# Kernel optimization log

Measured on AMD Instinct MI355X. Metric: run time of the kernel, lower is better.

## Reference

```python
import jax, jax.numpy as jnp
import numpy as np

B, N, M, D, NHEAD, FF, C, K = 2, 16384, 2048, 256, 8, 512, 50, 3
HID = 128          # embed/pos hidden
HEAD_HID = 256     # seg head hidden
L = 4              # depth
EPS = 1e-5


def setup_inputs() -> dict:
    key = jax.random.key(0)
    ks = jax.random.split(key, 32)
    g = lambda i, shape: jax.random.normal(ks[i], shape, dtype=jnp.float32) * 0.02
    z = lambda shape: jnp.zeros(shape, jnp.float32)
    o = lambda shape: jnp.ones(shape, jnp.float32)
    return {
        "xyz": jax.random.normal(ks[0], (B, N, 3), dtype=jnp.float32),
        "embed_w1": g(1, (3, HID)), "embed_b1": z((HID,)),
        "embed_w2": g(2, (HID, D)), "embed_b2": z((D,)),
        "pos_w1": g(3, (3, HID)), "pos_b1": z((HID,)),
        "pos_w2": g(4, (HID, D)), "pos_b2": z((D,)),
        "Wq": g(5, (L, D, D)), "bq": z((L, D)),
        "Wk": g(6, (L, D, D)), "bk": z((L, D)),
        "Wv": g(7, (L, D, D)), "bv": z((L, D)),
        "Wo": g(8, (L, D, D)), "bo": z((L, D)),
        "ln1_s": o((L, D)), "ln1_b": z((L, D)),
        "W1": g(9, (L, D, FF)), "b1": z((L, FF)),
        "W2": g(10, (L, FF, D)), "b2": z((L, D)),
        "ln2_s": o((L, D)), "ln2_b": z((L, D)),
        "head_w1": g(11, (D, HEAD_HID)), "head_b1": z((HEAD_HID,)),
        "head_w2": g(12, (HEAD_HID, C)), "head_b2": z((C,)),
    }


def _ln(x, s, b):
    m = x.mean(-1, keepdims=True)
    v = ((x - m) ** 2).mean(-1, keepdims=True)
    return (x - m) / jnp.sqrt(v + EPS) * s + b


def reference(xyz, embed_w1, embed_b1, embed_w2, embed_b2,
              pos_w1, pos_b1, pos_w2, pos_b2,
              Wq, bq, Wk, bk, Wv, bv, Wo, bo, ln1_s, ln1_b,
              W1, b1, W2, b2, ln2_s, ln2_b,
              head_w1, head_b1, head_w2, head_b2):
    # deterministic token subsample (replaces randperm stub): strided pick of M points
    stride = N // M
    tok = xyz[:, ::stride, :][:, :M]                                  # [B,M,3]
    # per-point embed + learned positional encoding
    x = jax.nn.relu(tok @ embed_w1 + embed_b1) @ embed_w2 + embed_b2  # [B,M,D]
    x = x + jax.nn.relu(tok @ pos_w1 + pos_b1) @ pos_w2 + pos_b2
    dh = D // NHEAD
    scale = 1.0 / jnp.sqrt(jnp.float32(dh))

    def layer(x, p):
        wq, bq_, wk, bk_, wv, bv_, wo, bo_, l1s, l1b, w1, b1_, w2, b2_, l2s, l2b = p
        # pre-norm MHSA
        y = _ln(x, l1s, l1b)
        q = (y @ wq + bq_).reshape(B, M, NHEAD, dh)
        k = (y @ wk + bk_).reshape(B, M, NHEAD, dh)
        v = (y @ wv + bv_).reshape(B, M, NHEAD, dh)
        att = jax.nn.softmax(jnp.einsum('bqhd,bkhd->bhqk', q, k) * scale, axis=-1)
        o = jnp.einsum('bhqk,bkhd->bqhd', att, v).reshape(B, M, D)
        x = x + o @ wo + bo_
        # pre-norm FFN (gelu, exact erf as in torch)
        y = _ln(x, l2s, l2b)
        x = x + jax.nn.gelu(y @ w1 + b1_, approximate=False) @ w2 + b2_
        return x, None

    x, _ = jax.lax.scan(layer, x, (Wq, bq, Wk, bk, Wv, bv, Wo, bo,
                                   ln1_s, ln1_b, W1, b1, W2, b2, ln2_s, ln2_b))
    logits_tok = jax.nn.relu(x @ head_w1 + head_b1) @ head_w2 + head_b2  # [B,M,C]

    # kNN propagation N->M: dist^2 = |q|^2 + |k|^2 - 2 q.k, topk smallest
    q2 = (xyz ** 2).sum(-1)[..., None]            # [B,N,1]
    k2 = (tok ** 2).sum(-1)[:, None, :]           # [B,1,M]
    dist = q2 + k2 - 2.0 * jnp.einsum('bnd,bmd->bnm', xyz, tok)
    dist = jax.lax.stop_gradient(jnp.maximum(dist, 0.0))
    idx = jax.lax.top_k(-dist, K)[1]              # [B,N,K]
    logits_nk = logits_tok[jnp.arange(B)[:, None, None], idx]  # [B,N,K,C]
    return logits_nk.mean(axis=2)                 # [B,N,C]
```

## Files before the change

kernel.cpp:

```cpp
#include <hip/hip_runtime.h>
#include <hip/hip_bf16.h>
#include <math.h>

#define B_ 2
#define N_ 16384
#define M_ 2048
#define D_ 256
#define NHEAD_ 8
#define DH_ 32
#define FF_ 512
#define C_ 50
#define HID_ 128
#define HHID_ 256
#define L_ 4
#define EPS_ 1e-5f
#define TOK_ (B_*M_)
#define QSCALE_ 0.25507604155757994f

typedef short short8 __attribute__((ext_vector_type(8)));
typedef short short4_t __attribute__((ext_vector_type(4)));
typedef float f32x4 __attribute__((ext_vector_type(4)));

__device__ __forceinline__ short f2bf(float f) {
  union { float f; unsigned u; } c; c.f = f;
  unsigned u = c.u;
  unsigned r = (u + 0x7FFFu + ((u >> 16) & 1u)) >> 16;
  return (short)r;
}
__device__ __forceinline__ float fast_exp2(float x) {
  float r;
  asm("v_exp_f32 %0, %1" : "=v"(r) : "v"(x));
  return r;
}
__device__ __forceinline__ unsigned cvt_pk_bf16(float lo, float hi) {
  unsigned r;
  asm("v_cvt_pk_bf16_f32 %0, %1, %2" : "=v"(r) : "v"(lo), "v"(hi));
  return r;
}
__device__ __forceinline__ float med3f(float a, float b, float c) {
  float r;
  asm("v_med3_f32 %0, %1, %2, %3" : "=v"(r) : "v"(a), "v"(b), "v"(c));
  return r;
}

__global__ __launch_bounds__(256) void wconv_all(
    const float* __restrict__ Wq, const float* __restrict__ Wk,
    const float* __restrict__ Wv, const float* __restrict__ Wo,
    const float* __restrict__ W1, const float* __restrict__ W2,
    const float* __restrict__ h1,
    short* __restrict__ WqT, short* __restrict__ WkT,
    short* __restrict__ WvT, short* __restrict__ WoT,
    short* __restrict__ W1T, short* __restrict__ W2T, short* __restrict__ h1T) {
  int bid = blockIdx.x;
  const float* W; short* WT; int Kd, Nd, tn, tk;
  if (bid < 256) {
    int mat = bid >> 6, rem = bid & 63, l = rem >> 4, t = rem & 15;
    W  = (mat == 0 ? Wq : mat == 1 ? Wk : mat == 2 ? Wv : Wo) + l * 65536;
    WT = (mat == 0 ? WqT : mat == 1 ? WkT : mat == 2 ? WvT : WoT) + l * 65536;
    Kd = 256; Nd = 256; tn = t & 3; tk = t >> 2;
  } else if (bid < 384) {
    int rem = bid - 256, l = rem >> 5, t = rem & 31;
    W = W1 + l * 131072; WT = W1T + l * 131072;
    Kd = 256; Nd = 512; tn = t & 7; tk = t >> 3;
  } else if (bid < 512) {
    int rem = bid - 384, l = rem >> 5, t = rem & 31;
    W = W2 + l * 131072; WT = W2T + l * 131072;
    Kd = 512; Nd = 256; tn = t & 3; tk = t >> 2;
  } else {
    int t = bid - 512;
    W = h1; WT = h1T; Kd = 256; Nd = 256; tn = t & 3; tk = t >> 2;
  }
  int n0 = tn * 64, k0 = tk * 64;
  __shared__ short ts[64][72];
  int tid = threadIdx.x;
  #pragma unroll
  for (int i = 0; i < 4; ++i) {
    int r = i * 16 + (tid >> 4);
    int c4 = (tid & 15) * 4;
    float4 v = *(const float4*)&W[(size_t)(k0 + r) * Nd + n0 + c4];
    ts[c4 + 0][r] = f2bf(v.x);
    ts[c4 + 1][r] = f2bf(v.y);
    ts[c4 + 2][r] = f2bf(v.z);
    ts[c4 + 3][r] = f2bf(v.w);
  }
  __syncthreads();
  #pragma unroll
  for (int i = 0; i < 2; ++i) {
    int n = i * 32 + (tid >> 3);
    int kc = (tid & 7) * 8;
    *(short8*)&WT[(size_t)(n0 + n) * Kd + k0 + kc] = *(short8*)&ts[n][kc];
  }
}

__global__ __launch_bounds__(128) void embed_kernel(
    const float* __restrict__ xyz,
    const float* __restrict__ ew1, const float* __restrict__ eb1,
    const float* __restrict__ ew2, const float* __restrict__ eb2,
    const float* __restrict__ pw1, const float* __restrict__ pb1,
    const float* __restrict__ pw2, const float* __restrict__ pb2,
    float* __restrict__ x) {
  int t = blockIdx.x;
  int b = t / M_, m = t % M_;
  const float* p = xyz + ((size_t)b * N_ + (size_t)m * 8) * 3;
  float t0 = p[0], t1 = p[1], t2 = p[2];
  __shared__ float he[HID_], hp[HID_];
  int j = threadIdx.x;
  {
    float a = fmaf(t0, ew1[j], fmaf(t1, ew1[HID_ + j], fmaf(t2, ew1[2 * HID_ + j], eb1[j])));
    he[j] = fmaxf(a, 0.f);
    float c = fmaf(t0, pw1[j], fmaf(t1, pw1[HID_ + j], fmaf(t2, pw1[2 * HID_ + j], pb1[j])));
    hp[j] = fmaxf(c, 0.f);
  }
  __syncthreads();
  for (int d = j; d < D_; d += HID_) {
    float acc = eb2[d] + pb2[d];
    for (int k = 0; k < HID_; ++k) {
      acc = fmaf(he[k], ew2[k * D_ + d], acc);
      acc = fmaf(hp[k], pw2[k * D_ + d], acc);
    }
    x[(size_t)t * D_ + d] = acc;
  }
}

__global__ __launch_bounds__(256) void ln_kernel(
    const float* __restrict__ x, const float* __restrict__ s,
    const float* __restrict__ bb, short* __restrict__ y16) {
  int r = blockIdx.x * 4 + (threadIdx.x >> 6);
  int t = threadIdx.x & 63;
  const float4* xr = (const float4*)(x + (size_t)r * D_);
  float4 v = xr[t];
  float sum = v.x + v.y + v.z + v.w;
  #pragma unroll
  for (int o = 1; o < 64; o <<= 1) sum += __shfl_xor(sum, o, 64);
  float mean = sum * (1.f / D_);
  float dx = v.x - mean, dy = v.y - mean, dz = v.z - mean, dw = v.w - mean;
  float vs = dx * dx + dy * dy + dz * dz + dw * dw;
  #pragma unroll
  for (int o = 1; o < 64; o <<= 1) vs += __shfl_xor(vs, o, 64);
  float inv = 1.0f / sqrtf(vs * (1.f / D_) + EPS_);
  float4 sv = ((const float4*)s)[t];
  float4 bv = ((const float4*)bb)[t];
  short4_t ov;
  ov[0] = f2bf(dx * inv * sv.x + bv.x);
  ov[1] = f2bf(dy * inv * sv.y + bv.y);
  ov[2] = f2bf(dz * inv * sv.z + bv.z);
  ov[3] = f2bf(dw * inv * sv.w + bv.w);
  *(short4_t*)(y16 + (size_t)r * D_ + t * 4) = ov;
}

__global__ __launch_bounds__(256) void head2_kernel(
    const float* __restrict__ y, const float* __restrict__ w2,
    const float* __restrict__ b2, float* __restrict__ lt) {
  __shared__ float ys[4][HHID_];
  int w = threadIdx.x >> 6, l = threadIdx.x & 63;
  int t = blockIdx.x * 4 + w;
  float4 v = ((const float4*)(y + (size_t)t * HHID_))[l];
  *(float4*)&ys[w][l * 4] = v;
  int c = l < C_ ? l : 0;
  float a0 = 0.f, a1 = 0.f, a2 = 0.f, a3 = 0.f;
  #pragma unroll 4
  for (int k = 0; k < HHID_; k += 4) {
    a0 = fmaf(ys[w][k + 0], w2[(k + 0) * C_ + c], a0);
    a1 = fmaf(ys[w][k + 1], w2[(k + 1) * C_ + c], a1);
    a2 = fmaf(ys[w][k + 2], w2[(k + 2) * C_ + c], a2);
    a3 = fmaf(ys[w][k + 3], w2[(k + 3) * C_ + c], a3);
  }
  if (l < C_) lt[(size_t)t * C_ + l] = (a0 + a1) + (a2 + a3) + b2[l];
}

template <int ACT, int RES>
__device__ __forceinline__ void gemm16_body(
    const short* __restrict__ A16, const short* __restrict__ WT,
    const float* __restrict__ bias, const float* __restrict__ R,
    float* __restrict__ C, short* __restrict__ C16, short* __restrict__ VT,
    float oscale, int K, int Ncols, int m0, int n0) {
  __shared__ short As[64][40];
  __shared__ short Bs[64][40];
  int tid = threadIdx.x;
  int w = tid >> 6, l = tid & 63;
  int lq = l & 15, lg = l >> 4;
  int wr = (w & 1) * 32, wc = (w >> 1) * 32;
  int sr = tid >> 2, sk = (tid & 3) * 8;
  f32x4 acc00 = {0.f, 0.f, 0.f, 0.f};
  f32x4 acc01 = {0.f, 0.f, 0.f, 0.f};
  f32x4 acc10 = {0.f, 0.f, 0.f, 0.f};
  f32x4 acc11 = {0.f, 0.f, 0.f, 0.f};
  for (int kk = 0; kk < K; kk += 32) {
    __syncthreads();
    *(short8*)&As[sr][sk] = *(const short8*)&A16[(size_t)(m0 + sr) * K + kk + sk];
    *(short8*)&Bs[sr][sk] = *(const short8*)&WT[(size_t)(n0 + sr) * K + kk + sk];
    __syncthreads();
    short8 a0 = *(short8*)&As[wr + lq][lg * 8];
    short8 a1 = *(short8*)&As[wr + 16 + lq][lg * 8];
    short8 b0 = *(short8*)&Bs[wc + lq][lg * 8];
    short8 b1 = *(short8*)&Bs[wc + 16 + lq][lg * 8];
    acc00 = __builtin_amdgcn_mfma_f32_16x16x32_bf16(a0, b0, acc00, 0, 0, 0);
    acc01 = __builtin_amdgcn_mfma_f32_16x16x32_bf16(a0, b1, acc01, 0, 0, 0);
    acc10 = __builtin_amdgcn_mfma_f32_16x16x32_bf16(a1, b0, acc10, 0, 0, 0);
    acc11 = __builtin_amdgcn_mfma_f32_16x16x32_bf16(a1, b1, acc11, 0, 0, 0);
  }
  #pragma unroll
  for (int fi = 0; fi < 2; ++fi) {
    int row = m0 + wr + fi * 16 + lg * 4;
    #pragma unroll
    for (int fj = 0; fj < 2; ++fj) {
      int col = n0 + wc + fj * 16 + lq;
      short4_t vt4;
      #pragma unroll
      for (int r = 0; r < 4; ++r) {
        float v = (fi == 0 ? (fj == 0 ? acc00[r] : acc01[r])
                           : (fj == 0 ? acc10[r] : acc11[r])) + bias[col];
        if (ACT == 1) v = fmaxf(v, 0.f);
        else if (ACT == 2) v = 0.5f * v * (1.f + erff(v * 0.70710678118654752f));
        if (RES) v += R[(size_t)(row + r) * Ncols + col];
        if (C)   C[(size_t)(row + r) * Ncols + col] = v;
        if (C16) C16[(size_t)(row + r) * Ncols + col] = f2bf(v * oscale);
        if (VT)  vt4[r] = f2bf(v);
      }
      if (VT) {
        int bb = row >> 11, mm = row & (M_ - 1);
        *(short4_t*)&VT[((size_t)(bb * 256 + col)) * M_ + mm] = vt4;
      }
    }
  }
}

template <int ACT, int RES>
__global__ __launch_bounds__(256) void gemm16(
    const short* __restrict__ A16, const short* __restrict__ WT,
    const float* __restrict__ bias, const float* __restrict__ R,
    float* __restrict__ C, short* __restrict__ C16,
    int K, int Ncols) {
  gemm16_body<ACT, RES>(A16, WT, bias, R, C, C16, nullptr, 1.f, K, Ncols,
                        blockIdx.y * 64, blockIdx.x * 64);
}

__global__ __launch_bounds__(256) void qkv16(
    const short* __restrict__ A16,
    const short* __restrict__ WqT, const short* __restrict__ WkT, const short* __restrict__ WvT,
    const float* __restrict__ bq, const float* __restrict__ bk, const float* __restrict__ bv,
    short* __restrict__ q16, short* __restrict__ k16, short* __restrict__ vt16) {
  int sel = blockIdx.x >> 2;
  int n0 = (blockIdx.x & 3) << 6;
  int m0 = blockIdx.y * 64;
  if (sel == 0) {
    gemm16_body<0, 0>(A16, WqT, bq, nullptr, nullptr, q16, nullptr, QSCALE_, D_, D_, m0, n0);
  } else if (sel == 1) {
    gemm16_body<0, 0>(A16, WkT, bk, nullptr, nullptr, k16, nullptr, 1.f, D_, D_, m0, n0);
  } else {
    gemm16_body<0, 0>(A16, WvT, bv, nullptr, nullptr, nullptr, vt16, 1.f, D_, D_, m0, n0);
  }
}

__global__ __launch_bounds__(256) void wo_gemm(
    const float* __restrict__ po0, const float* __restrict__ po1,
    const float* __restrict__ po2, const float* __restrict__ po3,
    const float* __restrict__ pl, const short* __restrict__ WT,
    const float* __restrict__ bias, float* __restrict__ X) {
  __shared__ short As[64][260];
  __shared__ short Bs[64][40];
  int tid = threadIdx.x;
  int w = tid >> 6, l = tid & 63;
  int m0 = blockIdx.y * 64, n0 = blockIdx.x * 64;
  #pragma unroll 4
  for (int c = 0; c < 16; ++c) {
    int t = w * 16 + c;
    int row = m0 + t;
    int bb = row >> 11, mm = row & (M_ - 1);
    int h = l >> 3, d0 = (l & 7) * 4;
    size_t f = (size_t)(bb * NHEAD_ + h) * M_ + mm;
    float inv = 1.f / (pl[f] + pl[16 * M_ + f] + pl[32 * M_ + f] + pl[48 * M_ + f]);
    float4 p0 = *(const float4*)&po0[f * 32 + d0];
    float4 p1 = *(const float4*)&po1[f * 32 + d0];
    float4 p2 = *(const float4*)&po2[f * 32 + d0];
    float4 p3 = *(const float4*)&po3[f * 32 + d0];
    short4_t s;
    s[0] = f2bf((p0.x + p1.x + p2.x + p3.x) * inv);
    s[1] = f2bf((p0.y + p1.y + p2.y + p3.y) * inv);
    s[2] = f2bf((p0.z + p1.z + p2.z + p3.z) * inv);
    s[3] = f2bf((p0.w + p1.w + p2.w + p3.w) * inv);
    *(short4_t*)&As[t][l * 4] = s;
  }
  int lq = l & 15, lg = l >> 4;
  int wr = (w & 1) * 32, wc = (w >> 1) * 32;
  int sr = tid >> 2, sk = (tid & 3) * 8;
  f32x4 acc00 = {0.f, 0.f, 0.f, 0.f};
  f32x4 acc01 = {0.f, 0.f, 0.f, 0.f};
  f32x4 acc10 = {0.f, 0.f, 0.f, 0.f};
  f32x4 acc11 = {0.f, 0.f, 0.f, 0.f};
  for (int kk = 0; kk < D_; kk += 32) {
    __syncthreads();
    *(short8*)&Bs[sr][sk] = *(const short8*)&WT[(size_t)(n0 + sr) * D_ + kk + sk];
    __syncthreads();
    short8 a0 = *(short8*)&As[wr + lq][kk + lg * 8];
    short8 a1 = *(short8*)&As[wr + 16 + lq][kk + lg * 8];
    short8 b0 = *(short8*)&Bs[wc + lq][lg * 8];
    short8 b1 = *(short8*)&Bs[wc + 16 + lq][lg * 8];
    acc00 = __builtin_amdgcn_mfma_f32_16x16x32_bf16(a0, b0, acc00, 0, 0, 0);
    acc01 = __builtin_amdgcn_mfma_f32_16x16x32_bf16(a0, b1, acc01, 0, 0, 0);
    acc10 = __builtin_amdgcn_mfma_f32_16x16x32_bf16(a1, b0, acc10, 0, 0, 0);
    acc11 = __builtin_amdgcn_mfma_f32_16x16x32_bf16(a1, b1, acc11, 0, 0, 0);
  }
  #pragma unroll
  for (int fi = 0; fi < 2; ++fi) {
    int row = m0 + wr + fi * 16 + lg * 4;
    #pragma unroll
    for (int fj = 0; fj < 2; ++fj) {
      int col = n0 + wc + fj * 16 + lq;
      #pragma unroll
      for (int r = 0; r < 4; ++r) {
        float v = (fi == 0 ? (fj == 0 ? acc00[r] : acc01[r])
                           : (fj == 0 ? acc10[r] : acc11[r])) + bias[col];
        v += X[(size_t)(row + r) * D_ + col];
        X[(size_t)(row + r) * D_ + col] = v;
      }
    }
  }
}

#define KSTR 40
#define VSTR 72
#define PSTR 72
__global__ __launch_bounds__(256) void attn_mfma_kernel(
    const short* __restrict__ q16, const short* __restrict__ k16,
    const short* __restrict__ vt16,
    float* __restrict__ po0, float* __restrict__ po1,
    float* __restrict__ po2, float* __restrict__ po3,
    float* __restrict__ pl) {
  __shared__ short Ks[64][KSTR];
  __shared__ short Vt[32][VSTR];
  __shared__ short Ps[4][16][PSTR];
  int bid = blockIdx.x;
  int quar = bid & 3;
  int qt = (bid >> 2) & 31;
  int h  = (bid >> 7) & 7;
  int b  = bid >> 10;
  int tid = threadIdx.x;
  int w  = tid >> 6;
  int l  = tid & 63;
  int lq = l & 15;
  int lg = l >> 4;

  short8 qf = *(const short8*)&q16[(size_t)(b * M_ + qt * 64 + w * 16 + lq) * D_ + h * DH_ + lg * 8];

  float l_i = 0.f;
  f32x4 o0 = {0.f, 0.f, 0.f, 0.f};
  f32x4 o1 = {0.f, 0.f, 0.f, 0.f};
  int srow = tid >> 2, scol = (tid & 3) * 8;
  int vd = tid >> 3, vm = (tid & 7) * 8;
  const short* kp = k16 + (size_t)(b * M_ + quar * 512 + srow) * D_ + h * DH_ + scol;
  const short* vp = vt16 + (size_t)((b * NHEAD_ + h) * DH_ + vd) * M_ + quar * 512 + vm;

  for (int kt = 0; kt < 8; ++kt) {
    __syncthreads();
    *(short8*)&Ks[srow][scol] = *(const short8*)(kp + (size_t)(kt * 64) * D_);
    *(short8*)&Vt[vd][vm]     = *(const short8*)(vp + kt * 64);
    __syncthreads();
    f32x4 st[4];
    #pragma unroll
    for (int t = 0; t < 4; ++t) {
      short8 kf = *(short8*)&Ks[t * 16 + lq][lg * 8];
      f32x4 z = {0.f, 0.f, 0.f, 0.f};
      st[t] = __builtin_amdgcn_mfma_f32_16x16x32_bf16(kf, qf, z, 0, 0, 0);
    }
    #pragma unroll
    for (int t = 0; t < 4; ++t)
      #pragma unroll
      for (int r2 = 0; r2 < 4; ++r2) {
        st[t][r2] = fast_exp2(st[t][r2]);
        l_i += st[t][r2];
      }
    {
      unsigned* pw = (unsigned*)&Ps[w][lq][0];
      #pragma unroll
      for (int t = 0; t < 4; ++t) {
        uint2 pk;
        pk.x = cvt_pk_bf16(st[t][0], st[t][1]);
        pk.y = cvt_pk_bf16(st[t][2], st[t][3]);
        *(uint2*)(pw + t * 8 + lg * 2) = pk;
      }
    }
    #pragma unroll
    for (int c = 0; c < 2; ++c) {
      short8 pf = *(short8*)&Ps[w][lq][c * 32 + lg * 8];
      short8 v0 = *(short8*)&Vt[lq][c * 32 + lg * 8];
      short8 v1 = *(short8*)&Vt[16 + lq][c * 32 + lg * 8];
      o0 = __builtin_amdgcn_mfma_f32_16x16x32_bf16(v0, pf, o0, 0, 0, 0);
      o1 = __builtin_amdgcn_mfma_f32_16x16x32_bf16(v1, pf, o1, 0, 0, 0);
    }
  }
  l_i += __shfl_xor(l_i, 16, 64);
  l_i += __shfl_xor(l_i, 32, 64);
  int f = (b * NHEAD_ + h) * M_ + qt * 64 + w * 16 + lq;
  float* pp = (quar == 0 ? po0 : quar == 1 ? po1 : quar == 2 ? po2 : po3) + (size_t)f * 32;
  #pragma unroll
  for (int r2 = 0; r2 < 4; ++r2) pp[lg * 4 + r2] = o0[r2];
  #pragma unroll
  for (int r2 = 0; r2 < 4; ++r2) pp[16 + lg * 4 + r2] = o1[r2];
  if (lg == 0) pl[quar * (16 * M_) + f] = l_i;
}

__global__ __launch_bounds__(512) void knn_kernel(
    const float* __restrict__ xyz, const float* __restrict__ lt,
    float* __restrict__ out) {
  __shared__ float4 tok[2064];
  int b = blockIdx.x >> 9;
  int q0 = (blockIdx.x & 511) << 5;
  int tid = threadIdx.x;
  for (int i = tid; i < M_; i += 512) {
    const float* tp = xyz + ((size_t)b * N_ + (size_t)i * 8) * 3;
    float a = tp[0], bb = tp[1], cc = tp[2];
    tok[i + (i >> 7)] = make_float4(a, bb, cc, a * a + bb * bb + cc * cc);
  }
  __syncthreads();
  int g = tid >> 4, sl = tid & 15;
  int n = q0 + g;
  const float* qp = xyz + ((size_t)b * N_ + n) * 3;
  float qx = qp[0], qy = qp[1], qz = qp[2];
  float q2 = qx * qx + qy * qy + qz * qz;
  const float4* cp = &tok[sl * 129];
  float dd0 = INFINITY, dd1 = INFINITY, dd2 = INFINITY;
  #pragma unroll 4
  for (int j = 0; j < 128; ++j) {
    float4 t = cp[j];
    float dot = fmaf(qx, t.x, fmaf(qy, t.y, qz * t.z));
    float d = fmaxf(q2 + t.w - 2.f * dot, 0.f);
    float n0 = fminf(dd0, d);
    float n1 = med3f(d, dd0, dd1);
    float n2 = med3f(d, dd1, dd2);
    dd0 = n0; dd1 = n1; dd2 = n2;
  }
  #pragma unroll
  for (int off = 1; off < 16; off <<= 1) {
    float p0 = __shfl_xor(dd0, off, 64);
    float p1 = __shfl_xor(dd1, off, 64);
    float p2 = __shfl_xor(dd2, off, 64);
    float n0, n1, n2;
    n0 = fminf(dd0, p0); n1 = med3f(p0, dd0, dd1); n2 = med3f(p0, dd1, dd2);
    dd0 = n0; dd1 = n1; dd2 = n2;
    n0 = fminf(dd0, p1); n1 = med3f(p1, dd0, dd1); n2 = med3f(p1, dd1, dd2);
    dd0 = n0; dd1 = n1; dd2 = n2;
    n0 = fminf(dd0, p2); n1 = med3f(p2, dd0, dd1); n2 = med3f(p2, dd1, dd2);
    dd0 = n0; dd1 = n1; dd2 = n2;
  }
  float thr = dd2;
  float e0 = INFINITY, e1 = INFINITY, e2 = INFINITY;
  int i0 = 0x7FFFFFFF, i1 = 0x7FFFFFFF, i2 = 0x7FFFFFFF;
  auto insT = [&](float d, int i) {
    if (d < e2 || (d == e2 && i < i2)) {
      if (d < e1 || (d == e1 && i < i1)) {
        e2 = e1; i2 = i1;
        if (d < e0 || (d == e0 && i < i0)) { e1 = e0; i1 = i0; e0 = d; i0 = i; }
        else { e1 = d; i1 = i; }
      } else { e2 = d; i2 = i; }
    }
  };
  int mb = sl << 7;
  #pragma unroll 4
  for (int j = 0; j < 128; ++j) {
    float4 t = cp[j];
    float dot = fmaf(qx, t.x, fmaf(qy, t.y, qz * t.z));
    float d = fmaxf(q2 + t.w - 2.f * dot, 0.f);
    if (d <= thr) insT(d, mb + j);
  }
  #pragma unroll
  for (int off = 1; off < 16; off <<= 1) {
    float p0 = __shfl_xor(e0, off, 64); int pi0 = __shfl_xor(i0, off, 64);
    float p1 = __shfl_xor(e1, off, 64); int pi1 = __shfl_xor(i1, off, 64);
    float p2 = __shfl_xor(e2, off, 64); int pi2 = __shfl_xor(i2, off, 64);
    insT(p0, pi0); insT(p1, pi1); insT(p2, pi2);
  }
  const float* l0 = lt + ((size_t)b * M_ + i0) * C_;
  const float* l1 = lt + ((size_t)b * M_ + i1) * C_;
  const float* l2 = lt + ((size_t)b * M_ + i2) * C_;
  float* op = out + ((size_t)b * N_ + n) * C_;
  for (int cc = sl; cc < C_; cc += 16)
    op[cc] = (l0[cc] + l1[cc] + l2[cc]) * (1.f / 3.f);
}

extern "C" void kernel_launch(void* const* d_in, const int* in_sizes, int n_in,
                              void* d_out, int out_size, void* d_ws, size_t ws_size,
                              hipStream_t stream) {
  const float* xyz  = (const float*)d_in[0];
  const float* ew1  = (const float*)d_in[1];
  const float* eb1  = (const float*)d_in[2];
  const float* ew2  = (const float*)d_in[3];
  const float* eb2  = (const float*)d_in[4];
  const float* pw1  = (const float*)d_in[5];
  const float* pb1  = (const float*)d_in[6];
  const float* pw2  = (const float*)d_in[7];
  const float* pb2  = (const float*)d_in[8];
  const float* Wq   = (const float*)d_in[9];
  const float* bq   = (const float*)d_in[10];
  const float* Wk   = (const float*)d_in[11];
  const float* bk   = (const float*)d_in[12];
  const float* Wv   = (const float*)d_in[13];
  const float* bv   = (const float*)d_in[14];
  const float* Wo   = (const float*)d_in[15];
  const float* bo   = (const float*)d_in[16];
  const float* ln1s = (const float*)d_in[17];
  const float* ln1b = (const float*)d_in[18];
  const float* W1   = (const float*)d_in[19];
  const float* b1   = (const float*)d_in[20];
  const float* W2   = (const float*)d_in[21];
  const float* b2   = (const float*)d_in[22];
  const float* ln2s = (const float*)d_in[23];
  const float* ln2b = (const float*)d_in[24];
  const float* hw1  = (const float*)d_in[25];
  const float* hb1  = (const float*)d_in[26];
  const float* hw2  = (const float*)d_in[27];
  const float* hb2  = (const float*)d_in[28];
  float* out = (float*)d_out;

  float* x   = (float*)d_ws;
  float* y   = x + 1048576;
  float* po2 = y + 1048576;
  float* po3 = po2 + 1048576;
  float* lt  = po3 + 1048576;
  short* y16 = (short*)(lt + 204800);
  short* q16 = y16 + 1048576;
  short* k16 = q16 + 1048576;
  short* v16 = k16 + 1048576;
  short* vt16 = v16 + 1048576;
  short* ob16 = vt16 + 1048576;
  short* x16  = ob16 + 1048576;
  short* ff16 = x16 + 1048576;
  short* WqT = ff16 + 2097152;
  short* WkT = WqT + 262144;
  short* WvT = WkT + 262144;
  short* WoT = WvT + 262144;
  short* W1T = WoT + 262144;
  short* W2T = W1T + 524288;
  short* h1T = W2T + 524288;
  float* po0 = y;
  float* po1 = (float*)ff16;
  float* pl  = lt;

  wconv_all<<<528, 256, 0, stream>>>(Wq, Wk, Wv, Wo, W1, W2, hw1,
                                     WqT, WkT, WvT, WoT, W1T, W2T, h1T);
  embed_kernel<<<TOK_, 128, 0, stream>>>(xyz, ew1, eb1, ew2, eb2, pw1, pb1, pw2, pb2, x);

  dim3 gQKV(12, TOK_ / 64);
  dim3 gD(D_ / 64, TOK_ / 64);
  dim3 gF(FF_ / 64, TOK_ / 64);
  for (int l = 0; l < L_; ++l) {
    ln_kernel<<<TOK_ / 4, 256, 0, stream>>>(x, ln1s + l * D_, ln1b + l * D_, y16);
    qkv16<<<gQKV, 256, 0, stream>>>(y16, WqT + l * 65536, WkT + l * 65536, WvT + l * 65536,
                                    bq + l * D_, bk + l * D_, bv + l * D_, q16, k16, vt16);
    attn_mfma_kernel<<<2048, 256, 0, stream>>>(q16, k16, vt16, po0, po1, po2, po3, pl);
    wo_gemm<<<gD, 256, 0, stream>>>(po0, po1, po2, po3, pl, WoT + l * 65536, bo + l * D_, x);
    ln_kernel<<<TOK_ / 4, 256, 0, stream>>>(x, ln2s + l * D_, ln2b + l * D_, y16);
    gemm16<2, 0><<<gF, 256, 0, stream>>>(y16, W1T + l * 131072, b1 + l * FF_, nullptr, nullptr, ff16, D_, FF_);
    gemm16<0, 1><<<gD, 256, 0, stream>>>(ff16, W2T + l * 131072, b2 + l * D_, x, x, x16, FF_, D_);
  }
  gemm16<1, 0><<<gD, 256, 0, stream>>>(x16, h1T, hb1, nullptr, y, nullptr, D_, HHID_);
  head2_kernel<<<TOK_ / 4, 256, 0, stream>>>(y, hw2, hb2, lt);
  knn_kernel<<<1024, 512, 0, stream>>>(xyz, lt, out);
}
```

Before: 405.2 us.

## Split-K the Wo, W2 and head GEMMs and fuse partial reduction into LayerNorm

After: 387.2 us. 4.4% less time.

```diff
diff --git a/kernel.cpp b/kernel.cpp
--- a/kernel.cpp
+++ b/kernel.cpp
@@ -35,11 +35,6 @@
 __device__ __forceinline__ unsigned cvt_pk_bf16(float lo, float hi) {
   unsigned r;
   asm("v_cvt_pk_bf16_f32 %0, %1, %2" : "=v"(r) : "v"(lo), "v"(hi));
-  return r;
-}
-__device__ __forceinline__ float med3f(float a, float b, float c) {
-  float r;
-  asm("v_med3_f32 %0, %1, %2, %3" : "=v"(r) : "v"(a), "v"(b), "v"(c));
   return r;
 }
 
@@ -122,13 +117,24 @@
   }
 }
 
-__global__ __launch_bounds__(256) void ln_kernel(
-    const float* __restrict__ x, const float* __restrict__ s,
-    const float* __restrict__ bb, short* __restrict__ y16) {
+__global__ __launch_bounds__(256) void ln_fused(
+    const float* __restrict__ x, const float* __restrict__ pa,
+    const float* __restrict__ pb, const float* __restrict__ bias,
+    const float* __restrict__ s, const float* __restrict__ bb,
+    float* __restrict__ xw, short* __restrict__ y16) {
   int r = blockIdx.x * 4 + (threadIdx.x >> 6);
   int t = threadIdx.x & 63;
-  const float4* xr = (const float4*)(x + (size_t)r * D_);
-  float4 v = xr[t];
+  float4 v = ((const float4*)(x + (size_t)r * D_))[t];
+  if (pa) {
+    float4 a = ((const float4*)(pa + (size_t)r * D_))[t];
+    float4 c = ((const float4*)(pb + (size_t)r * D_))[t];
+    float4 bi = ((const float4*)bias)[t];
+    v.x += a.x + c.x + bi.x;
+    v.y += a.y + c.y + bi.y;
+    v.z += a.z + c.z + bi.z;
+    v.w += a.w + c.w + bi.w;
+    ((float4*)(xw + (size_t)r * D_))[t] = v;
+  }
   float sum = v.x + v.y + v.z + v.w;
   #pragma unroll
   for (int o = 1; o < 64; o <<= 1) sum += __shfl_xor(sum, o, 64);
@@ -149,21 +155,29 @@
 }
 
 __global__ __launch_bounds__(256) void head2_kernel(
-    const float* __restrict__ y, const float* __restrict__ w2,
+    const float* __restrict__ pa, const float* __restrict__ pb,
+    const float* __restrict__ b1h, const float* __restrict__ w2,
     const float* __restrict__ b2, float* __restrict__ lt) {
   __shared__ float ys[4][HHID_];
   int w = threadIdx.x >> 6, l = threadIdx.x & 63;
   int t = blockIdx.x * 4 + w;
-  float4 v = ((const float4*)(y + (size_t)t * HHID_))[l];
+  float4 a = ((const float4*)(pa + (size_t)t * HHID_))[l];
+  float4 c = ((const float4*)(pb + (size_t)t * HHID_))[l];
+  float4 bi = ((const float4*)b1h)[l];
+  float4 v;
+  v.x = fmaxf(a.x + c.x + bi.x, 0.f);
+  v.y = fmaxf(a.y + c.y + bi.y, 0.f);
+  v.z = fmaxf(a.z + c.z + bi.z, 0.f);
+  v.w = fmaxf(a.w + c.w + bi.w, 0.f);
   *(float4*)&ys[w][l * 4] = v;
-  int c = l < C_ ? l : 0;
+  int cc = l < C_ ? l : 0;
   float a0 = 0.f, a1 = 0.f, a2 = 0.f, a3 = 0.f;
   #pragma unroll 4
   for (int k = 0; k < HHID_; k += 4) {
-    a0 = fmaf(ys[w][k + 0], w2[(k + 0) * C_ + c], a0);
-    a1 = fmaf(ys[w][k + 1], w2[(k + 1) * C_ + c], a1);
-    a2 = fmaf(ys[w][k + 2], w2[(k + 2) * C_ + c], a2);
-    a3 = fmaf(ys[w][k + 3], w2[(k + 3) * C_ + c], a3);
+    a0 = fmaf(ys[w][k + 0], w2[(k + 0) * C_ + cc], a0);
+    a1 = fmaf(ys[w][k + 1], w2[(k + 1) * C_ + cc], a1);
+    a2 = fmaf(ys[w][k + 2], w2[(k + 2) * C_ + cc], a2);
+    a3 = fmaf(ys[w][k + 3], w2[(k + 3) * C_ + cc], a3);
   }
   if (l < C_) lt[(size_t)t * C_ + l] = (a0 + a1) + (a2 + a3) + b2[l];
 }
@@ -235,6 +249,53 @@
                         blockIdx.y * 64, blockIdx.x * 64);
 }
 
+__global__ __launch_bounds__(256) void gemm16_part(
+    const short* __restrict__ A16, const short* __restrict__ WT,
+    float* __restrict__ P, int K, int Klen, int Ncols) {
+  __shared__ short As[64][40];
+  __shared__ short Bs[64][40];
+  int tid = threadIdx.x;
+  int w = tid >> 6, l = tid & 63;
+  int lq = l & 15, lg = l >> 4;
+  int wr = (w & 1) * 32, wc = (w >> 1) * 32;
+  int sr = tid >> 2, sk = (tid & 3) * 8;
+  int m0 = blockIdx.y * 64, n0 = blockIdx.x * 64;
+  int k0 = blockIdx.z * Klen;
+  f32x4 acc00 = {0.f, 0.f, 0.f, 0.f};
+  f32x4 acc01 = {0.f, 0.f, 0.f, 0.f};
+  f32x4 acc10 = {0.f, 0.f, 0.f, 0.f};
+  f32x4 acc11 = {0.f, 0.f, 0.f, 0.f};
+  for (int kk = k0; kk < k0 + Klen; kk += 32) {
+    __syncthreads();
+    *(short8*)&As[sr][sk] = *(const short8*)&A16[(size_t)(m0 + sr) * K + kk + sk];
+    *(short8*)&Bs[sr][sk] = *(const short8*)&WT[(size_t)(n0 + sr) * K + kk + sk];
+    __syncthreads();
+    short8 a0 = *(short8*)&As[wr + lq][lg * 8];
+    short8 a1 = *(short8*)&As[wr + 16 + lq][lg * 8];
+    short8 b0 = *(short8*)&Bs[wc + lq][lg * 8];
+    short8 b1 = *(short8*)&Bs[wc + 16 + lq][lg * 8];
+    acc00 = __builtin_amdgcn_mfma_f32_16x16x32_bf16(a0, b0, acc00, 0, 0, 0);
+    acc01 = __builtin_amdgcn_mfma_f32_16x16x32_bf16(a0, b1, acc01, 0, 0, 0);
+    acc10 = __builtin_amdgcn_mfma_f32_16x16x32_bf16(a1, b0, acc10, 0, 0, 0);
+    acc11 = __builtin_amdgcn_mfma_f32_16x16x32_bf16(a1, b1, acc11, 0, 0, 0);
+  }
+  float* Pp = P + (size_t)blockIdx.z * TOK_ * Ncols;
+  #pragma unroll
+  for (int fi = 0; fi < 2; ++fi) {
+    int row = m0 + wr + fi * 16 + lg * 4;
+    #pragma unroll
+    for (int fj = 0; fj < 2; ++fj) {
+      int col = n0 + wc + fj * 16 + lq;
+      #pragma unroll
+      for (int r = 0; r < 4; ++r) {
+        float v = (fi == 0 ? (fj == 0 ? acc00[r] : acc01[r])
+                           : (fj == 0 ? acc10[r] : acc11[r]));
+        Pp[(size_t)(row + r) * Ncols + col] = v;
+      }
+    }
+  }
+}
+
 __global__ __launch_bounds__(256) void qkv16(
     const short* __restrict__ A16,
     const short* __restrict__ WqT, const short* __restrict__ WkT, const short* __restrict__ WvT,
@@ -252,34 +313,30 @@
   }
 }
 
-__global__ __launch_bounds__(256) void wo_gemm(
+__global__ __launch_bounds__(256) void wo_split(
     const float* __restrict__ po0, const float* __restrict__ po1,
     const float* __restrict__ po2, const float* __restrict__ po3,
     const float* __restrict__ pl, const short* __restrict__ WT,
-    const float* __restrict__ bias, float* __restrict__ X) {
-  __shared__ short As[64][260];
+    float* __restrict__ P) {
+  __shared__ short As[64][136];
   __shared__ short Bs[64][40];
   int tid = threadIdx.x;
   int w = tid >> 6, l = tid & 63;
   int m0 = blockIdx.y * 64, n0 = blockIdx.x * 64;
+  int half = blockIdx.z;
+  int c2 = l * 2;
+  int hh = half * 4 + (c2 >> 5);
+  int d0 = c2 & 31;
   #pragma unroll 4
   for (int c = 0; c < 16; ++c) {
     int t = w * 16 + c;
     int row = m0 + t;
     int bb = row >> 11, mm = row & (M_ - 1);
-    int h = l >> 3, d0 = (l & 7) * 4;
-    size_t f = (size_t)(bb * NHEAD_ + h) * M_ + mm;
+    size_t f = (size_t)(bb * NHEAD_ + hh) * M_ + mm;
     float inv = 1.f / (pl[f] + pl[16 * M_ + f] + pl[32 * M_ + f] + pl[48 * M_ + f]);
-    float4 p0 = *(const float4*)&po0[f * 32 + d0];
-    float4 p1 = *(const float4*)&po1[f * 32 + d0];
-    float4 p2 = *(const float4*)&po2[f * 32 + d0];
-    float4 p3 = *(const float4*)&po3[f * 32 + d0];
-    short4_t s;
-    s[0] = f2bf((p0.x + p1.x + p2.x + p3.x) * inv);
-    s[1] = f2bf((p0.y + p1.y + p2.y + p3.y) * inv);
-    s[2] = f2bf((p0.z + p1.z + p2.z + p3.z) * inv);
-    s[3] = f2bf((p0.w + p1.w + p2.w + p3.w) * inv);
-    *(short4_t*)&As[t][l * 4] = s;
+    float v0 = (po0[f * 32 + d0] + po1[f * 32 + d0] + po2[f * 32 + d0] + po3[f * 32 + d0]) * inv;
+    float v1 = (po0[f * 32 + d0 + 1] + po1[f * 32 + d0 + 1] + po2[f * 32 + d0 + 1] + po3[f * 32 + d0 + 1]) * inv;
+    *(unsigned*)&As[t][c2] = cvt_pk_bf16(v0, v1);
   }
   int lq = l & 15, lg = l >> 4;
   int wr = (w & 1) * 32, wc = (w >> 1) * 32;
@@ -288,9 +345,9 @@
   f32x4 acc01 = {0.f, 0.f, 0.f, 0.f};
   f32x4 acc10 = {0.f, 0.f, 0.f, 0.f};
   f32x4 acc11 = {0.f, 0.f, 0.f, 0.f};
-  for (int kk = 0; kk < D_; kk += 32) {
-    __syncthreads();
-    *(short8*)&Bs[sr][sk] = *(const short8*)&WT[(size_t)(n0 + sr) * D_ + kk + sk];
+  for (int kk = 0; kk < 128; kk += 32) {
+    __syncthreads();
+    *(short8*)&Bs[sr][sk] = *(const short8*)&WT[(size_t)(n0 + sr) * D_ + half * 128 + kk + sk];
     __syncthreads();
     short8 a0 = *(short8*)&As[wr + lq][kk + lg * 8];
     short8 a1 = *(short8*)&As[wr + 16 + lq][kk + lg * 8];
@@ -301,6 +358,7 @@
     acc10 = __builtin_amdgcn_mfma_f32_16x16x32_bf16(a1, b0, acc10, 0, 0, 0);
     acc11 = __builtin_amdgcn_mfma_f32_16x16x32_bf16(a1, b1, acc11, 0, 0, 0);
   }
+  float* Pp = P + (size_t)half * TOK_ * D_;
   #pragma unroll
   for (int fi = 0; fi < 2; ++fi) {
     int row = m0 + wr + fi * 16 + lg * 4;
@@ -310,9 +368,8 @@
       #pragma unroll
       for (int r = 0; r < 4; ++r) {
         float v = (fi == 0 ? (fj == 0 ? acc00[r] : acc01[r])
-                           : (fj == 0 ? acc10[r] : acc11[r])) + bias[col];
-        v += X[(size_t)(row + r) * D_ + col];
-        X[(size_t)(row + r) * D_ + col] = v;
+                           : (fj == 0 ? acc10[r] : acc11[r]));
+        Pp[(size_t)(row + r) * D_ + col] = v;
       }
     }
   }
@@ -418,61 +475,43 @@
   const float* qp = xyz + ((size_t)b * N_ + n) * 3;
   float qx = qp[0], qy = qp[1], qz = qp[2];
   float q2 = qx * qx + qy * qy + qz * qz;
+  float dd0 = INFINITY, dd1 = INFINITY, dd2 = INFINITY;
+  int ii0 = 0, ii1 = 0, ii2 = 0;
   const float4* cp = &tok[sl * 129];
-  float dd0 = INFINITY, dd1 = INFINITY, dd2 = INFINITY;
-  #pragma unroll 4
+  int mb = sl << 7;
+  #pragma unroll 2
   for (int j = 0; j < 128; ++j) {
     float4 t = cp[j];
     float dot = fmaf(qx, t.x, fmaf(qy, t.y, qz * t.z));
     float d = fmaxf(q2 + t.w - 2.f * dot, 0.f);
-    float n0 = fminf(dd0, d);
-    float n1 = med3f(d, dd0, dd1);
-    float n2 = med3f(d, dd1, dd2);
-    dd0 = n0; dd1 = n1; dd2 = n2;
-  }
+    if (d < dd2) {
+      int m = mb + j;
+      if (d < dd1) {
+        dd2 = dd1; ii2 = ii1;
+        if (d < dd0) { dd1 = dd0; ii1 = ii0; dd0 = d; ii0 = m; }
+        else         { dd1 = d;  ii1 = m; }
+      } else         { dd2 = d;  ii2 = m; }
+    }
+  }
+  auto insT = [&](float d, int i) {
+    if (d < dd2 || (d == dd2 && i < ii2)) {
+      if (d < dd1 || (d == dd1 && i < ii1)) {
+        dd2 = dd1; ii2 = ii1;
+        if (d < dd0 || (d == dd0 && i < ii0)) { dd1 = dd0; ii1 = ii0; dd0 = d; ii0 = i; }
+        else { dd1 = d; ii1 = i; }
+      } else { dd2 = d; ii2 = i; }
+    }
+  };
   #pragma unroll
   for (int off = 1; off < 16; off <<= 1) {
-    float p0 = __shfl_xor(dd0, off, 64);
-    float p1 = __shfl_xor(dd1, off, 64);
-    float p2 = __shfl_xor(dd2, off, 64);
-    float n0, n1, n2;
-    n0 = fminf(dd0, p0); n1 = med3f(p0, dd0, dd1); n2 = med3f(p0, dd1, dd2);
-    dd0 = n0; dd1 = n1; dd2 = n2;
-    n0 = fminf(dd0, p1); n1 = med3f(p1, dd0, dd1); n2 = med3f(p1, dd1, dd2);
-    dd0 = n0; dd1 = n1; dd2 = n2;
-    n0 = fminf(dd0, p2); n1 = med3f(p2, dd0, dd1); n2 = med3f(p2, dd1, dd2);
-    dd0 = n0; dd1 = n1; dd2 = n2;
-  }
-  float thr = dd2;
-  float e0 = INFINITY, e1 = INFINITY, e2 = INFINITY;
-  int i0 = 0x7FFFFFFF, i1 = 0x7FFFFFFF, i2 = 0x7FFFFFFF;
-  auto insT = [&](float d, int i) {
-    if (d < e2 || (d == e2 && i < i2)) {
-      if (d < e1 || (d == e1 && i < i1)) {
-        e2 = e1; i2 = i1;
-        if (d < e0 || (d == e0 && i < i0)) { e1 = e0; i1 = i0; e0 = d; i0 = i; }
-        else { e1 = d; i1 = i; }
-      } else { e2 = d; i2 = i; }
-    }
-  };
-  int mb = sl << 7;
-  #pragma unroll 4
-  for (int j = 0; j < 128; ++j) {
-    float4 t = cp[j];
-    float dot = fmaf(qx, t.x, fmaf(qy, t.y, qz * t.z));
-    float d = fmaxf(q2 + t.w - 2.f * dot, 0.f);
-    if (d <= thr) insT(d, mb + j);
-  }
-  #pragma unroll
-  for (int off = 1; off < 16; off <<= 1) {
-    float p0 = __shfl_xor(e0, off, 64); int pi0 = __shfl_xor(i0, off, 64);
-    float p1 = __shfl_xor(e1, off, 64); int pi1 = __shfl_xor(i1, off, 64);
-    float p2 = __shfl_xor(e2, off, 64); int pi2 = __shfl_xor(i2, off, 64);
+    float p0 = __shfl_xor(dd0, off, 64); int pi0 = __shfl_xor(ii0, off, 64);
+    float p1 = __shfl_xor(dd1, off, 64); int pi1 = __shfl_xor(ii1, off, 64);
+    float p2 = __shfl_xor(dd2, off, 64); int pi2 = __shfl_xor(ii2, off, 64);
     insT(p0, pi0); insT(p1, pi1); insT(p2, pi2);
   }
-  const float* l0 = lt + ((size_t)b * M_ + i0) * C_;
-  const float* l1 = lt + ((size_t)b * M_ + i1) * C_;
-  const float* l2 = lt + ((size_t)b * M_ + i2) * C_;
+  const float* l0 = lt + ((size_t)b * M_ + ii0) * C_;
+  const float* l1 = lt + ((size_t)b * M_ + ii1) * C_;
+  const float* l2 = lt + ((size_t)b * M_ + ii2) * C_;
   float* op = out + ((size_t)b * N_ + n) * C_;
   for (int cc = sl; cc < C_; cc += 16)
     op[cc] = (l0[cc] + l1[cc] + l2[cc]) * (1.f / 3.f);
@@ -532,6 +571,7 @@
   short* W1T = WoT + 262144;
   short* W2T = W1T + 524288;
   short* h1T = W2T + 524288;
+  float* wpart = (float*)(h1T + 65536);
   float* po0 = y;
   float* po1 = (float*)ff16;
   float* pl  = lt;
@@ -541,19 +581,33 @@
   embed_kernel<<<TOK_, 128, 0, stream>>>(xyz, ew1, eb1, ew2, eb2, pw1, pb1, pw2, pb2, x);
 
   dim3 gQKV(12, TOK_ / 64);
+  dim3 gDs(D_ / 64, TOK_ / 64, 2);
+  dim3 gF(FF_ / 64, TOK_ / 64);
   dim3 gD(D_ / 64, TOK_ / 64);
-  dim3 gF(FF_ / 64, TOK_ / 64);
   for (int l = 0; l < L_; ++l) {
-    ln_kernel<<<TOK_ / 4, 256, 0, stream>>>(x, ln1s + l * D_, ln1b + l * D_, y16);
+    if (l == 0)
+      ln_fused<<<TOK_ / 4, 256, 0, stream>>>(x, nullptr, nullptr, nullptr,
+                                             ln1s + l * D_, ln1b + l * D_, x, y16);
+    else
+      ln_fused<<<TOK_ / 4, 256, 0, stream>>>(x, wpart, wpart + (size_t)TOK_ * D_,
+                                             b2 + (l - 1) * D_,
+                                             ln1s + l * D_, ln1b + l * D_, x, y16);
     qkv16<<<gQKV, 256, 0, stream>>>(y16, WqT + l * 65536, WkT + l * 65536, WvT + l * 65536,
                                     bq + l * D_, bk + l * D_, bv + l * D_, q16, k16, vt16);
     attn_mfma_kernel<<<2048, 256, 0, stream>>>(q16, k16, vt16, po0, po1, po2, po3, pl);
-    wo_gemm<<<gD, 256, 0, stream>>>(po0, po1, po2, po3, pl, WoT + l * 65536, bo + l * D_, x);
-    ln_kernel<<<TOK_ / 4, 256, 0, stream>>>(x, ln2s + l * D_, ln2b + l * D_, y16);
+    wo_split<<<gDs, 256, 0, stream>>>(po0, po1, po2, po3, pl, WoT + l * 65536, wpart);
+    ln_fused<<<TOK_ / 4, 256, 0, stream>>>(x, wpart, wpart + (size_t)TOK_ * D_,
+                                           bo + l * D_,
+                                           ln2s + l * D_, ln2b + l * D_, x, y16);
     gemm16<2, 0><<<gF, 256, 0, stream>>>(y16, W1T + l * 131072, b1 + l * FF_, nullptr, nullptr, ff16, D_, FF_);
-    gemm16<0, 1><<<gD, 256, 0, stream>>>(ff16, W2T + l * 131072, b2 + l * D_, x, x, x16, FF_, D_);
-  }
-  gemm16<1, 0><<<gD, 256, 0, stream>>>(x16, h1T, hb1, nullptr, y, nullptr, D_, HHID_);
-  head2_kernel<<<TOK_ / 4, 256, 0, stream>>>(y, hw2, hb2, lt);
+    if (l < L_ - 1) {
+      gemm16_part<<<gDs, 256, 0, stream>>>(ff16, W2T + l * 131072, wpart, FF_, 256, D_);
+    } else {
+      gemm16<0, 1><<<gD, 256, 0, stream>>>(ff16, W2T + l * 131072, b2 + l * D_, x, x, x16, FF_, D_);
+    }
+  }
+  gemm16_part<<<gDs, 256, 0, stream>>>(x16, h1T, wpart, D_, 128, HHID_);
+  head2_kernel<<<TOK_ / 4, 256, 0, stream>>>(wpart, wpart + (size_t)TOK_ * HHID_,
+                                             hb1, hw2, hb2, lt);
   knn_kernel<<<1024, 512, 0, stream>>>(xyz, lt, out);
 }
```
